# Kernel optimization log

Hardware: AMD Instinct MI355X
Metric: run time of the kernel (lower is better)

Reference implementation:

```python
import jax, jax.numpy as jnp
import numpy as np

B, L, D, H = 2, 2048, 2048, 16
HD = D // H  # head_dim = 128
EPS = 1e-5


def setup_inputs() -> dict:
    key = jax.random.key(0)
    ks = jax.random.split(key, 5)
    return {
        "x": jax.random.normal(ks[0], (B, L, D), dtype=jnp.float32),
        "Wq": jax.random.normal(ks[1], (D, D), dtype=jnp.float32) * (D ** -0.5),
        "Wk": jax.random.normal(ks[2], (D, D), dtype=jnp.float32) * (D ** -0.5),
        "Wv": jax.random.normal(ks[3], (D, D), dtype=jnp.float32) * (D ** -0.5),
        "gamma_logit": jax.random.normal(ks[4], (H,), dtype=jnp.float32),
        "gn_weight": jnp.ones((D,), dtype=jnp.float32),
        "gn_bias": jnp.zeros((D,), dtype=jnp.float32),
    }


def reference(x, Wq, Wk, Wv, gamma_logit, gn_weight, gn_bias):
    scale = HD ** -0.5
    # projections (torch Linear: y = x @ W.T)
    Q = jnp.einsum('bld,ed->ble', x, Wq).reshape(B, L, H, HD).transpose(0, 2, 1, 3)
    K = jnp.einsum('bld,ed->ble', x, Wk).reshape(B, L, H, HD).transpose(0, 2, 1, 3)
    V = jnp.einsum('bld,ed->ble', x, Wv).reshape(B, L, H, HD).transpose(0, 2, 1, 3)
    # causal exponential decay matrix D[h,i,j] = gamma_h^(i-j), lower-triangular
    pos = jnp.arange(L)
    dist = jnp.abs(pos[None, :] - pos[:, None]).astype(jnp.float32)  # [L,L]
    gamma = jax.nn.sigmoid(gamma_logit)  # [H]
    Dmat = jnp.tril(gamma[:, None, None] ** dist[None, :, :])  # [H,L,L]
    # decayed linear attention (no softmax)
    attn = jnp.einsum('bhid,bhjd->bhij', Q, K) * scale * Dmat[None]
    out = jnp.einsum('bhij,bhje->bhie', attn, V)  # [B,H,L,HD]
    out = out.transpose(0, 2, 1, 3)  # [B,L,H,HD]
    # GroupNorm: channels=D, groups=H, spatial=L -> normalize per (b,h) over (L,HD)
    mean = out.mean(axis=(1, 3), keepdims=True)
    var = out.var(axis=(1, 3), keepdims=True)
    y = (out - mean) * jax.lax.rsqrt(var + EPS)
    y = y * gn_weight.reshape(1, 1, H, HD) + gn_bias.reshape(1, 1, H, HD)
    return y.reshape(B, L, D)
```

## Files before the change

kernel.cpp:

```cpp
#include <hip/hip_runtime.h>
#include <hip/hip_bf16.h>
#include <math.h>

#define B_  2
#define L_  2048
#define D_  2048
#define H_  16
#define HD_ 128
#define EPS_ 1e-5f

typedef __attribute__((ext_vector_type(8)))  short short8;
typedef __attribute__((ext_vector_type(4)))  float f32x4;
typedef __attribute__((ext_vector_type(16))) float f32x16;

static __device__ inline unsigned short bfb(float x) {
    __hip_bfloat16 h = __float2bfloat16(x);
    unsigned short s;
    __builtin_memcpy(&s, &h, 2);
    return s;
}
static __device__ inline unsigned pk2(float a, float b) {
    return (unsigned)bfb(a) | ((unsigned)bfb(b) << 16);
}
static __device__ inline float bf2f(unsigned short u) {
    unsigned v = ((unsigned)u) << 16;
    float f;
    __builtin_memcpy(&f, &v, 4);
    return f;
}

static __device__ __forceinline__ void gld_lds16(const void* g, void* l) {
    __builtin_amdgcn_global_load_lds(
        (const __attribute__((address_space(1))) unsigned int*)g,
        (__attribute__((address_space(3))) unsigned int*)l,
        16, 0, 0);
}

#define XN4 2097152
#define WN4 1048576
#define TOT4 (XN4 + 3 * WN4)

__global__ __launch_bounds__(256) void cast4_kernel(
    const float* __restrict__ x,  const float* __restrict__ Wq,
    const float* __restrict__ Wk, const float* __restrict__ Wv,
    __hip_bfloat16* __restrict__ dst)
{
    int i = blockIdx.x * 256 + threadIdx.x;
    const int st = gridDim.x * 256;
    for (; i < TOT4; i += st) {
        const float* s;
        int off;
        if (i < XN4)                { s = x;  off = i; }
        else if (i < XN4 + WN4)     { s = Wq; off = i - XN4; }
        else if (i < XN4 + 2 * WN4) { s = Wk; off = i - XN4 - WN4; }
        else                        { s = Wv; off = i - XN4 - 2 * WN4; }
        float4 v = ((const float4*)s)[off];
        uint2 r;
        r.x = pk2(v.x, v.y);
        r.y = pk2(v.z, v.w);
        ((uint2*)dst)[i] = r;
    }
}

__global__ __launch_bounds__(256) void proj_bf16(
    const __hip_bfloat16* __restrict__ X,
    const __hip_bfloat16* __restrict__ Wqb, const __hip_bfloat16* __restrict__ Wkb,
    const __hip_bfloat16* __restrict__ Wvb,
    __hip_bfloat16* __restrict__ Qo, __hip_bfloat16* __restrict__ Ko,
    __hip_bfloat16* __restrict__ Vt, __hip_bfloat16* __restrict__ Kt)
{
    const __hip_bfloat16* W = (blockIdx.z == 0) ? Wqb : (blockIdx.z == 1 ? Wkb : Wvb);
    __hip_bfloat16*       O = (blockIdx.z == 0) ? Qo  : (blockIdx.z == 1 ? Ko  : Vt);

    __shared__ __align__(16) char Al[128 * 64 * 2];
    __shared__ __align__(16) char Bl[128 * 64 * 2];

    const int t  = threadIdx.x;
    const int w  = t >> 6, l = t & 63;
    const int li = l & 15, hi4 = l >> 4;
    const int wr = w >> 1, wcn = w & 1;
    const int m0 = blockIdx.y * 128;
    const int n0 = blockIdx.x * 128;

    const int srow = l >> 3;
    const int scol = ((l & 7) ^ (l >> 3)) * 8;

    f32x4 acc[4][4];
    #pragma unroll
    for (int i = 0; i < 4; ++i)
        #pragma unroll
        for (int j = 0; j < 4; ++j)
            #pragma unroll
            for (int r = 0; r < 4; ++r) acc[i][j][r] = 0.f;

    for (int k0 = 0; k0 < D_; k0 += 64) {
        if (k0) __syncthreads();
        #pragma unroll
        for (int c = 0; c < 4; ++c) {
            const int chunk = w * 4 + c;
            const int row   = chunk * 8 + srow;
            gld_lds16(X + (size_t)(m0 + row) * D_ + k0 + scol, Al + chunk * 1024);
            gld_lds16(W + (size_t)(n0 + row) * D_ + k0 + scol, Bl + chunk * 1024);
        }
        __syncthreads();

        #pragma unroll
        for (int s = 0; s < 2; ++s) {
            const int cbA = (s * 64 + hi4 * 16) ^ ((li & 7) << 4);
            short8 af[4], bf[4];
            #pragma unroll
            for (int mi = 0; mi < 4; ++mi)
                af[mi] = *(const short8*)(Al + (wr * 64 + mi * 16 + li) * 128 + cbA);
            #pragma unroll
            for (int ni = 0; ni < 4; ++ni)
                bf[ni] = *(const short8*)(Bl + (wcn * 64 + ni * 16 + li) * 128 + cbA);
            #pragma unroll
            for (int mi = 0; mi < 4; ++mi)
                #pragma unroll
                for (int ni = 0; ni < 4; ++ni)
                    acc[mi][ni] = __builtin_amdgcn_mfma_f32_16x16x32_bf16(
                        af[mi], bf[ni], acc[mi][ni], 0, 0, 0);
        }
    }

    if (blockIdx.z == 2) {
        #pragma unroll
        for (int mi = 0; mi < 4; ++mi) {
            #pragma unroll
            for (int ni = 0; ni < 4; ++ni) {
                const int n     = n0 + wcn * 64 + ni * 16 + li;
                const int mbase = m0 + wr * 64 + mi * 16 + hi4 * 4;
                const int b = mbase >> 11, ml = mbase & (L_ - 1);
                uint2 w2;
                w2.x = pk2(acc[mi][ni][0], acc[mi][ni][1]);
                w2.y = pk2(acc[mi][ni][2], acc[mi][ni][3]);
                *(uint2*)&O[((size_t)b * (H_ * HD_) + n) * L_ + ml] = w2;
            }
        }
    } else {
        #pragma unroll
        for (int mi = 0; mi < 4; ++mi) {
            #pragma unroll
            for (int ni = 0; ni < 4; ++ni) {
                const int n  = n0 + wcn * 64 + ni * 16 + li;
                const int h  = n >> 7, hd = n & (HD_ - 1);
                #pragma unroll
                for (int r = 0; r < 4; ++r) {
                    const int m = m0 + wr * 64 + mi * 16 + hi4 * 4 + r;
                    const int b = m >> 11, ml = m & (L_ - 1);
                    O[((size_t)(b * H_ + h) * L_ + ml) * HD_ + hd] =
                        __float2bfloat16(acc[mi][ni][r]);
                }
            }
        }
        if (blockIdx.z == 1 && Kt != nullptr) {
            #pragma unroll
            for (int mi = 0; mi < 4; ++mi) {
                #pragma unroll
                for (int ni = 0; ni < 4; ++ni) {
                    const int n     = n0 + wcn * 64 + ni * 16 + li;
                    const int mbase = m0 + wr * 64 + mi * 16 + hi4 * 4;
                    const int b = mbase >> 11, ml = mbase & (L_ - 1);
                    uint2 w2;
                    w2.x = pk2(acc[mi][ni][0], acc[mi][ni][1]);
                    w2.y = pk2(acc[mi][ni][2], acc[mi][ni][3]);
                    *(uint2*)&Kt[((size_t)b * (H_ * HD_) + n) * L_ + ml] = w2;
                }
            }
        }
    }
}

__global__ __launch_bounds__(256) void state_part(
    const __hip_bfloat16* __restrict__ KT, const __hip_bfloat16* __restrict__ VT,
    const float* __restrict__ gl, __hip_bfloat16* __restrict__ SpT)
{
    const int bid = blockIdx.x;
    const int bh  = bid & 31, c = bid >> 5;
    const int h   = bh & (H_ - 1);
    const int t   = threadIdx.x;
    const int w   = t >> 6, l = t & 63;
    const int li  = l & 31, hi = l >> 5;

    const float gamma = 1.f / (1.f + __expf(-gl[h]));
    const float lg2   = __log2f(gamma);

    __shared__ __align__(16) char Kl[32768];
    __shared__ __align__(16) char Vl[32768];

    const __hip_bfloat16* KTg = KT + (size_t)bh * (HD_ * L_);
    const __hip_bfloat16* VTg = VT + (size_t)bh * (HD_ * L_);
    const int gj = c * 128;
    const int srow4 = l >> 4, sslot = l & 15;

    #pragma unroll
    for (int cc = 0; cc < 8; ++cc) {
        const int ch = w * 8 + cc;
        const int r  = ch * 4 + srow4;
        const int sc = ((sslot ^ (r & 15)) * 8);
        gld_lds16(KTg + (size_t)r * L_ + gj + sc, Kl + ch * 1024);
        gld_lds16(VTg + (size_t)r * L_ + gj + sc, Vl + ch * 1024);
    }
    __syncthreads();

    f32x16 acc[4];
    #pragma unroll
    for (int cch = 0; cch < 4; ++cch)
        #pragma unroll
        for (int r = 0; r < 16; ++r) acc[cch][r] = 0.f;

    #pragma unroll
    for (int s = 0; s < 8; ++s) {
        const int boff = ((s * 2 + hi) ^ (li & 15)) << 4;
        short8 vraw = *(const short8*)(Vl + (w * 32 + li) * 256 + boff);
        short8 af;
        #pragma unroll
        for (int e = 0; e < 8; ++e) {
            const int jl = s * 16 + hi * 8 + e;
            const float f = bf2f((unsigned short)vraw[e]) *
                            exp2f(lg2 * (float)(127 - jl));
            af[e] = (short)bfb(f);
        }
        #pragma unroll
        for (int cch = 0; cch < 4; ++cch) {
            short8 bf = *(const short8*)(Kl + (cch * 32 + li) * 256 + boff);
            acc[cch] = __builtin_amdgcn_mfma_f32_32x32x16_bf16(af, bf, acc[cch], 0, 0, 0);
        }
    }

    __hip_bfloat16* Sp = SpT + (size_t)(bh * 16 + c) * 16384;
    #pragma unroll
    for (int cch = 0; cch < 4; ++cch)
        #pragma unroll
        for (int r = 0; r < 16; ++r) {
            const int d = w * 32 + (r & 3) + 8 * (r >> 2) + 4 * hi;
            Sp[(size_t)d * 128 + cch * 32 + li] = __float2bfloat16(acc[cch][r]);
        }
}

__global__ __launch_bounds__(256) void state_scan(
    const __hip_bfloat16* __restrict__ SpT, __hip_bfloat16* __restrict__ SbT,
    const float* __restrict__ gl)
{
    const int bh = blockIdx.x;
    const int h  = bh & (H_ - 1);
    const float gamma = 1.f / (1.f + __expf(-gl[h]));
    const float g128  = exp2f(__log2f(gamma) * 128.f);
    const int fid = blockIdx.y * 256 + threadIdx.x;

    float a0 = 0.f, a1 = 0.f, a2 = 0.f, a3 = 0.f;
    for (int c = 0; c < 16; ++c) {
        const size_t off = (size_t)(bh * 16 + c) * 16384 + (size_t)fid * 4;
        uint2 v = *(const uint2*)(SpT + off);
        a0 = g128 * a0 + bf2f((unsigned short)(v.x & 0xffff));
        a1 = g128 * a1 + bf2f((unsigned short)(v.x >> 16));
        a2 = g128 * a2 + bf2f((unsigned short)(v.y & 0xffff));
        a3 = g128 * a3 + bf2f((unsigned short)(v.y >> 16));
        uint2 o;
        o.x = pk2(a0, a1);
        o.y = pk2(a2, a3);
        *(uint2*)(SbT + off) = o;
    }
}

__global__ __launch_bounds__(256) void retn_kernel(
    const __hip_bfloat16* __restrict__ Qb, const __hip_bfloat16* __restrict__ Kb,
    const __hip_bfloat16* __restrict__ VT, const float* __restrict__ gl,
    float* __restrict__ out, float2* __restrict__ part,
    const __hip_bfloat16* __restrict__ SbT, int use_chunks)
{
    const int bid = blockIdx.x;
    const int mm  = bid >> 5;
    const int m   = use_chunks ? mm : ((mm < 8) ? (15 - mm) : (mm - 8));
    const int bh  = bid & 31;
    const int b   = bh >> 4, h = bh & (H_ - 1);
    const int t   = threadIdx.x;
    const int w   = t >> 6, l = t & 63;
    const int li  = l & 31, hi = l >> 5;

    const float gamma = 1.f / (1.f + __expf(-gl[h]));
    const float lg2   = __log2f(gamma);
    const float scale = 0.08838834764831845f;

    __shared__ __align__(16) char Klds[32768];
    __shared__ __align__(16) char Vlds[32768];
    __shared__ float rs[4], rq[4];

    const size_t base = (size_t)bh * (L_ * HD_);
    const __hip_bfloat16* VTg = VT + (size_t)bh * (HD_ * L_);
    const int i0 = m * 128 + w * 32;

    short8 qf[8];
    {
        const __hip_bfloat16* qrow = Qb + base + (size_t)(i0 + li) * HD_;
        #pragma unroll
        for (int s = 0; s < 8; ++s)
            qf[s] = *(const short8*)(qrow + s * 16 + hi * 8);
    }

    float df[16];
    #pragma unroll
    for (int r = 0; r < 16; ++r) {
        const int jl = (r & 3) + 8 * (r >> 2) + 4 * hi;
        df[r] = exp2f(lg2 * (float)(li - jl));
    }

    f32x16 acc[4];
    #pragma unroll
    for (int c = 0; c < 4; ++c)
        #pragma unroll
        for (int r = 0; r < 16; ++r) acc[c][r] = 0.f;

    const int srow4 = l >> 4;
    const int sslot = l & 15;

    if (use_chunks && m > 0) {
        const __hip_bfloat16* Sg = SbT + (size_t)(bh * 16 + (m - 1)) * 16384;
        #pragma unroll
        for (int cc = 0; cc < 8; ++cc) {
            const int ch = w * 8 + cc;
            const int r  = ch * 4 + srow4;
            const int sc = ((sslot ^ (r & 15)) * 8);
            gld_lds16(Sg + (size_t)r * 128 + sc, Klds + ch * 1024);
        }
        __syncthreads();
        #pragma unroll
        for (int s = 0; s < 8; ++s) {
            const int boff = ((s * 2 + hi) ^ (li & 15)) << 4;
            #pragma unroll
            for (int cch = 0; cch < 4; ++cch) {
                short8 sf = *(const short8*)(Klds + (cch * 32 + li) * 256 + boff);
                acc[cch] = __builtin_amdgcn_mfma_f32_32x32x16_bf16(
                    qf[s], sf, acc[cch], 0, 0, 0);
            }
        }
        #pragma unroll
        for (int r = 0; r < 16; ++r) {
            const int il = (r & 3) + 8 * (r >> 2) + 4 * hi + w * 32;
            const float fr = exp2f(lg2 * (float)(il + 1)) * scale;
            acc[0][r] *= fr; acc[1][r] *= fr; acc[2][r] *= fr; acc[3][r] *= fr;
        }
    }

    const int gj0 = use_chunks ? m * 128 : 0;
    for (int gj = gj0; gj <= m * 128; gj += 128) {
        __syncthreads();
        #pragma unroll
        for (int cc = 0; cc < 8; ++cc) {
            const int c  = w * 8 + cc;
            const int r  = c * 4 + srow4;
            const int sc = ((sslot ^ (r & 15)) * 8);
            gld_lds16(Kb + base + (size_t)(gj + r) * HD_ + sc, Klds + c * 1024);
            gld_lds16(VTg + (size_t)r * L_ + gj + sc,          Vlds + c * 1024);
        }
        __syncthreads();

        const int tmax = ((i0 - gj) >> 5) < 3 ? ((i0 - gj) >> 5) : 3;
        for (int jt = 0; jt <= tmax; ++jt) {
            const int j0 = gj + jt * 32;

            f32x16 c;
            #pragma unroll
            for (int r = 0; r < 16; ++r) c[r] = 0.f;
            #pragma unroll
            for (int s = 0; s < 8; ++s) {
                short8 kf = *(const short8*)(Klds + (jt * 32 + li) * 256 +
                                             (((s * 2 + hi) ^ (li & 15)) << 4));
                c = __builtin_amdgcn_mfma_f32_32x32x16_bf16(kf, qf[s], c, 0, 0, 0);
            }

            float p[16];
            const float bt = exp2f(lg2 * (float)(i0 - j0)) * scale;
            if (j0 == i0) {
                #pragma unroll
                for (int r = 0; r < 16; ++r) {
                    const int jl = (r & 3) + 8 * (r >> 2) + 4 * hi;
                    p[r] = (jl <= li) ? c[r] * (df[r] * bt) : 0.f;
                }
            } else {
                #pragma unroll
                for (int r = 0; r < 16; ++r) p[r] = c[r] * (df[r] * bt);
            }

            #pragma unroll
            for (int sl = 0; sl < 2; ++sl) {
                const int o = sl * 8;
                unsigned pk01 = pk2(p[o + 0], p[o + 1]);
                unsigned pk23 = pk2(p[o + 2], p[o + 3]);
                unsigned pk45 = pk2(p[o + 4], p[o + 5]);
                unsigned pk67 = pk2(p[o + 6], p[o + 7]);
                unsigned x01 = (unsigned)__shfl_xor((int)pk01, 32);
                unsigned x23 = (unsigned)__shfl_xor((int)pk23, 32);
                unsigned x45 = (unsigned)__shfl_xor((int)pk45, 32);
                unsigned x67 = (unsigned)__shfl_xor((int)pk67, 32);
                union { short8 v; unsigned u[4]; } pf;
                pf.u[0] = hi ? x45 : pk01;
                pf.u[1] = hi ? x67 : pk23;
                pf.u[2] = hi ? pk45 : x01;
                pf.u[3] = hi ? pk67 : x23;
                #pragma unroll
                for (int cch = 0; cch < 4; ++cch) {
                    short8 vf = *(const short8*)(Vlds + (cch * 32 + li) * 256 +
                                 (((jt * 4 + sl * 2 + hi) ^ (li & 15)) << 4));
                    acc[cch] = __builtin_amdgcn_mfma_f32_32x32x16_bf16(
                        pf.v, vf, acc[cch], 0, 0, 0);
                }
            }
        }
    }

    float s = 0.f, sq = 0.f;
    #pragma unroll
    for (int cch = 0; cch < 4; ++cch) {
        #pragma unroll
        for (int r = 0; r < 16; ++r) {
            const int row = (r & 3) + 8 * (r >> 2) + 4 * hi;
            const float v = acc[cch][r];
            out[(size_t)(b * L_ + i0 + row) * D_ + h * HD_ + cch * 32 + li] = v;
            s += v; sq += v * v;
        }
    }

    #pragma unroll
    for (int off = 32; off > 0; off >>= 1) {
        s  += __shfl_down(s, off);
        sq += __shfl_down(sq, off);
    }
    if (l == 0) { rs[w] = s; rq[w] = sq; }
    __syncthreads();
    if (t == 0)
        part[bh * 16 + m] = make_float2(rs[0] + rs[1] + rs[2] + rs[3],
                                        rq[0] + rq[1] + rq[2] + rq[3]);
}

__global__ __launch_bounds__(256) void gn_apply(
    float* __restrict__ out, const float2* __restrict__ part,
    const float* __restrict__ gw, const float* __restrict__ gb)
{
    const int bh = blockIdx.x, sl = blockIdx.y;
    const int b = bh >> 4, h = bh & (H_ - 1);
    const int t = threadIdx.x;

    float S = 0.f, SQ = 0.f;
    #pragma unroll
    for (int i = 0; i < 16; ++i) {
        float2 p = part[bh * 16 + i];
        S += p.x; SQ += p.y;
    }
    const float inv  = 1.f / (float)(L_ * HD_);
    const float mean = S * inv;
    float var = SQ * inv - mean * mean;
    if (var < 0.f) var = 0.f;
    const float rstd = rsqrtf(var + EPS_);

    #pragma unroll
    for (int it = 0; it < 4; ++it) {
        const int n  = it * 256 + t;
        const int ll = n >> 5, d4 = n & 31;
        const size_t idx = (size_t)(b * L_ + sl * 32 + ll) * D_ + h * HD_ + d4 * 4;
        float4 v = *(const float4*)&out[idx];
        const float4 w4 = *(const float4*)&gw[h * HD_ + d4 * 4];
        const float4 b4 = *(const float4*)&gb[h * HD_ + d4 * 4];
        v.x = (v.x - mean) * rstd * w4.x + b4.x;
        v.y = (v.y - mean) * rstd * w4.y + b4.y;
        v.z = (v.z - mean) * rstd * w4.z + b4.z;
        v.w = (v.w - mean) * rstd * w4.w + b4.w;
        *(float4*)&out[idx] = v;
    }
}

extern "C" void kernel_launch(void* const* d_in, const int* in_sizes, int n_in,
                              void* d_out, int out_size, void* d_ws, size_t ws_size,
                              hipStream_t stream) {
    const float* x  = (const float*)d_in[0];
    const float* Wq = (const float*)d_in[1];
    const float* Wk = (const float*)d_in[2];
    const float* Wv = (const float*)d_in[3];
    const float* gl = (const float*)d_in[4];
    const float* gw = (const float*)d_in[5];
    const float* gb = (const float*)d_in[6];
    float* out = (float*)d_out;

    __hip_bfloat16* ws = (__hip_bfloat16*)d_ws;
    __hip_bfloat16* xb  = ws;
    __hip_bfloat16* Wqb = xb  + 8388608;
    __hip_bfloat16* Wkb = Wqb + 4194304;
    __hip_bfloat16* Wvb = Wkb + 4194304;
    __hip_bfloat16* Qbf = Wvb + 4194304;
    __hip_bfloat16* Kbf = Qbf + 8388608;
    __hip_bfloat16* VTb = Kbf + 8388608;
    float2* part = (float2*)(VTb + 8388608);
    __hip_bfloat16* KTb = (__hip_bfloat16*)(part + 512);

    __hip_bfloat16* SpT = xb;
    __hip_bfloat16* SbT = Wqb;

    const int use_chunks = (ws_size >= 109056000ULL) ? 1 : 0;

    cast4_kernel<<<2048, 256, 0, stream>>>(x, Wq, Wk, Wv, xb);

    dim3 pgrid(D_ / 128, (B_ * L_) / 128, 3);
    proj_bf16<<<pgrid, 256, 0, stream>>>(xb, Wqb, Wkb, Wvb, Qbf, Kbf, VTb,
                                         use_chunks ? KTb : nullptr);

    if (use_chunks) {
        state_part<<<dim3(512), 256, 0, stream>>>(KTb, VTb, gl, SpT);
        state_scan<<<dim3(32, 16), 256, 0, stream>>>(SpT, SbT, gl);
    }

    retn_kernel<<<dim3(512), 256, 0, stream>>>(Qbf, Kbf, VTb, gl, out, part,
                                               use_chunks ? SbT : nullptr,
                                               use_chunks);

    gn_apply<<<dim3(32, 64), 256, 0, stream>>>(out, part, gw, gb);
}
```

Baseline: 189.1 us.

## Rewrite QKV projection as double-buffered 128x256 tile GEMM with interleaved prefetch

The projection kernel now runs as a single 1D grid of 768 blocks of 512 threads. Each block computes a 128x256 output tile over the concatenated Wq/Wk/Wv weights, which sit contiguously in the workspace. Tiles of the next two k-steps are loaded into double-buffered LDS while MFMAs run, using vmcnt waits, raw barriers and s_setprio. Blocks are remapped so neighbouring ones share weight tiles in cache. The aim is to hide global load latency and raise MFMA utilisation, at the cost of 96KB of LDS per block, which lowers occupancy.

```diff
diff --git a/kernel.cpp b/kernel.cpp
--- a/kernel.cpp
+++ b/kernel.cpp
@@ -8,6 +8,7 @@
 #define H_  16
 #define HD_ 128
 #define EPS_ 1e-5f
+#define NTK 32
 
 typedef __attribute__((ext_vector_type(8)))  short short8;
 typedef __attribute__((ext_vector_type(4)))  float f32x4;
@@ -62,28 +63,30 @@
     }
 }
 
-__global__ __launch_bounds__(256) void proj_bf16(
+__global__ __launch_bounds__(512) void proj8(
     const __hip_bfloat16* __restrict__ X,
-    const __hip_bfloat16* __restrict__ Wqb, const __hip_bfloat16* __restrict__ Wkb,
-    const __hip_bfloat16* __restrict__ Wvb,
+    const __hip_bfloat16* __restrict__ Wc,
     __hip_bfloat16* __restrict__ Qo, __hip_bfloat16* __restrict__ Ko,
-    __hip_bfloat16* __restrict__ Vt, __hip_bfloat16* __restrict__ Kt)
+    __hip_bfloat16* __restrict__ VT, __hip_bfloat16* __restrict__ KT)
 {
-    const __hip_bfloat16* W = (blockIdx.z == 0) ? Wqb : (blockIdx.z == 1 ? Wkb : Wvb);
-    __hip_bfloat16*       O = (blockIdx.z == 0) ? Qo  : (blockIdx.z == 1 ? Ko  : Vt);
-
-    __shared__ __align__(16) char Al[128 * 64 * 2];
-    __shared__ __align__(16) char Bl[128 * 64 * 2];
+    __shared__ __align__(16) char lds[98304];
 
     const int t  = threadIdx.x;
     const int w  = t >> 6, l = t & 63;
     const int li = l & 15, hi4 = l >> 4;
-    const int wr = w >> 1, wcn = w & 1;
-    const int m0 = blockIdx.y * 128;
-    const int n0 = blockIdx.x * 128;
+    const int wm = w >> 2, wn = w & 3;
+
+    const int bid = blockIdx.x;
+    const int wg  = (bid & 7) * 96 + (bid >> 3);
+    const int nt  = wg >> 5;
+    const int mt  = wg & 31;
+    const int m0  = mt * 128;
+    const int n0g = nt * 256;
 
     const int srow = l >> 3;
     const int scol = ((l & 7) ^ (l >> 3)) * 8;
+    const int ca0  = 2 * w;
+    const int cb0  = 4 * w;
 
     f32x4 acc[4][4];
     #pragma unroll
@@ -93,78 +96,136 @@
             #pragma unroll
             for (int r = 0; r < 4; ++r) acc[i][j][r] = 0.f;
 
-    for (int k0 = 0; k0 < D_; k0 += 64) {
-        if (k0) __syncthreads();
-        #pragma unroll
-        for (int c = 0; c < 4; ++c) {
-            const int chunk = w * 4 + c;
-            const int row   = chunk * 8 + srow;
-            gld_lds16(X + (size_t)(m0 + row) * D_ + k0 + scol, Al + chunk * 1024);
-            gld_lds16(W + (size_t)(n0 + row) * D_ + k0 + scol, Bl + chunk * 1024);
-        }
-        __syncthreads();
-
-        #pragma unroll
-        for (int s = 0; s < 2; ++s) {
-            const int cbA = (s * 64 + hi4 * 16) ^ ((li & 7) << 4);
-            short8 af[4], bf[4];
-            #pragma unroll
-            for (int mi = 0; mi < 4; ++mi)
-                af[mi] = *(const short8*)(Al + (wr * 64 + mi * 16 + li) * 128 + cbA);
-            #pragma unroll
-            for (int ni = 0; ni < 4; ++ni)
-                bf[ni] = *(const short8*)(Bl + (wcn * 64 + ni * 16 + li) * 128 + cbA);
-            #pragma unroll
-            for (int mi = 0; mi < 4; ++mi)
-                #pragma unroll
-                for (int ni = 0; ni < 4; ++ni)
-                    acc[mi][ni] = __builtin_amdgcn_mfma_f32_16x16x32_bf16(
-                        af[mi], bf[ni], acc[mi][ni], 0, 0, 0);
-        }
-    }
-
-    if (blockIdx.z == 2) {
-        #pragma unroll
-        for (int mi = 0; mi < 4; ++mi) {
-            #pragma unroll
-            for (int ni = 0; ni < 4; ++ni) {
-                const int n     = n0 + wcn * 64 + ni * 16 + li;
-                const int mbase = m0 + wr * 64 + mi * 16 + hi4 * 4;
+    auto STAGE_A = [&](int tt) {
+        char* Ab = lds + (tt & 1) * 16384;
+        char* Bb = lds + 32768 + (tt & 1) * 32768;
+        const size_t kc = (size_t)(tt * 64) + scol;
+        gld_lds16(X  + (size_t)(m0 + ca0 * 8 + srow) * D_ + kc,      Ab + ca0 * 1024);
+        gld_lds16(X  + (size_t)(m0 + ca0 * 8 + 8 + srow) * D_ + kc,  Ab + ca0 * 1024 + 1024);
+        gld_lds16(Wc + (size_t)(n0g + cb0 * 8 + srow) * D_ + kc,     Bb + cb0 * 1024);
+    };
+    auto STAGE_B = [&](int tt) {
+        char* Bb = lds + 32768 + (tt & 1) * 32768;
+        const size_t kc = (size_t)(tt * 64) + scol;
+        gld_lds16(Wc + (size_t)(n0g + (cb0 + 1) * 8 + srow) * D_ + kc, Bb + (cb0 + 1) * 1024);
+        gld_lds16(Wc + (size_t)(n0g + (cb0 + 2) * 8 + srow) * D_ + kc, Bb + (cb0 + 2) * 1024);
+        gld_lds16(Wc + (size_t)(n0g + (cb0 + 3) * 8 + srow) * D_ + kc, Bb + (cb0 + 3) * 1024);
+    };
+
+    STAGE_A(0); STAGE_B(0); STAGE_A(1); STAGE_B(1);
+
+    const int cbk0 = (hi4 * 16) ^ ((li & 7) << 4);
+    const int cbk1 = (64 + hi4 * 16) ^ ((li & 7) << 4);
+
+    #pragma unroll 2
+    for (int kt = 0; kt < NTK; ++kt) {
+        const char* Ab = lds + (kt & 1) * 16384;
+        const char* Bb = lds + 32768 + (kt & 1) * 32768;
+
+        if (kt < NTK - 1) asm volatile("s_waitcnt vmcnt(6)" ::: "memory");
+        else              asm volatile("s_waitcnt vmcnt(0)" ::: "memory");
+        __builtin_amdgcn_s_barrier();
+
+        short8 a0[4], b0[4], a1[4], b1[4];
+        #pragma unroll
+        for (int mf = 0; mf < 4; ++mf)
+            a0[mf] = *(const short8*)(Ab + (wm * 64 + mf * 16 + li) * 128 + cbk0);
+        #pragma unroll
+        for (int nf = 0; nf < 4; ++nf)
+            b0[nf] = *(const short8*)(Bb + (wn * 64 + nf * 16 + li) * 128 + cbk0);
+        __builtin_amdgcn_s_setprio(1);
+        #pragma unroll
+        for (int mf = 0; mf < 4; ++mf)
+            #pragma unroll
+            for (int nf = 0; nf < 2; ++nf)
+                acc[mf][nf] = __builtin_amdgcn_mfma_f32_16x16x32_bf16(
+                    a0[mf], b0[nf], acc[mf][nf], 0, 0, 0);
+        __builtin_amdgcn_s_setprio(0);
+
+        #pragma unroll
+        for (int mf = 0; mf < 4; ++mf)
+            a1[mf] = *(const short8*)(Ab + (wm * 64 + mf * 16 + li) * 128 + cbk1);
+        #pragma unroll
+        for (int nf = 0; nf < 4; ++nf)
+            b1[nf] = *(const short8*)(Bb + (wn * 64 + nf * 16 + li) * 128 + cbk1);
+        __builtin_amdgcn_s_setprio(1);
+        #pragma unroll
+        for (int mf = 0; mf < 4; ++mf)
+            #pragma unroll
+            for (int nf = 2; nf < 4; ++nf)
+                acc[mf][nf] = __builtin_amdgcn_mfma_f32_16x16x32_bf16(
+                    a0[mf], b0[nf], acc[mf][nf], 0, 0, 0);
+        __builtin_amdgcn_s_setprio(0);
+
+        asm volatile("s_waitcnt lgkmcnt(0)" ::: "memory");
+        __builtin_amdgcn_s_barrier();
+
+        if (kt < NTK - 2) STAGE_A(kt + 2);
+        __builtin_amdgcn_s_setprio(1);
+        #pragma unroll
+        for (int mf = 0; mf < 4; ++mf)
+            #pragma unroll
+            for (int nf = 0; nf < 2; ++nf)
+                acc[mf][nf] = __builtin_amdgcn_mfma_f32_16x16x32_bf16(
+                    a1[mf], b1[nf], acc[mf][nf], 0, 0, 0);
+        __builtin_amdgcn_s_setprio(0);
+
+        if (kt < NTK - 2) STAGE_B(kt + 2);
+        __builtin_amdgcn_s_setprio(1);
+        #pragma unroll
+        for (int mf = 0; mf < 4; ++mf)
+            #pragma unroll
+            for (int nf = 2; nf < 4; ++nf)
+                acc[mf][nf] = __builtin_amdgcn_mfma_f32_16x16x32_bf16(
+                    a1[mf], b1[nf], acc[mf][nf], 0, 0, 0);
+        __builtin_amdgcn_s_setprio(0);
+    }
+
+    const int zsel = n0g >> 11;
+    const int np   = n0g & (D_ - 1);
+    if (zsel == 2) {
+        #pragma unroll
+        for (int mf = 0; mf < 4; ++mf) {
+            #pragma unroll
+            for (int nf = 0; nf < 4; ++nf) {
+                const int n     = np + wn * 64 + nf * 16 + li;
+                const int mbase = m0 + wm * 64 + mf * 16 + hi4 * 4;
                 const int b = mbase >> 11, ml = mbase & (L_ - 1);
                 uint2 w2;
-                w2.x = pk2(acc[mi][ni][0], acc[mi][ni][1]);
-                w2.y = pk2(acc[mi][ni][2], acc[mi][ni][3]);
-                *(uint2*)&O[((size_t)b * (H_ * HD_) + n) * L_ + ml] = w2;
+                w2.x = pk2(acc[mf][nf][0], acc[mf][nf][1]);
+                w2.y = pk2(acc[mf][nf][2], acc[mf][nf][3]);
+                *(uint2*)&VT[((size_t)b * D_ + n) * L_ + ml] = w2;
             }
         }
     } else {
-        #pragma unroll
-        for (int mi = 0; mi < 4; ++mi) {
-            #pragma unroll
-            for (int ni = 0; ni < 4; ++ni) {
-                const int n  = n0 + wcn * 64 + ni * 16 + li;
+        __hip_bfloat16* O = zsel ? Ko : Qo;
+        #pragma unroll
+        for (int mf = 0; mf < 4; ++mf) {
+            #pragma unroll
+            for (int nf = 0; nf < 4; ++nf) {
+                const int n  = np + wn * 64 + nf * 16 + li;
                 const int h  = n >> 7, hd = n & (HD_ - 1);
                 #pragma unroll
                 for (int r = 0; r < 4; ++r) {
-                    const int m = m0 + wr * 64 + mi * 16 + hi4 * 4 + r;
+                    const int m = m0 + wm * 64 + mf * 16 + hi4 * 4 + r;
                     const int b = m >> 11, ml = m & (L_ - 1);
                     O[((size_t)(b * H_ + h) * L_ + ml) * HD_ + hd] =
-                        __float2bfloat16(acc[mi][ni][r]);
+                        __float2bfloat16(acc[mf][nf][r]);
                 }
             }
         }
-        if (blockIdx.z == 1 && Kt != nullptr) {
-            #pragma unroll
-            for (int mi = 0; mi < 4; ++mi) {
+        if (zsel == 1 && KT != nullptr) {
+            #pragma unroll
+            for (int mf = 0; mf < 4; ++mf) {
                 #pragma unroll
-                for (int ni = 0; ni < 4; ++ni) {
-                    const int n     = n0 + wcn * 64 + ni * 16 + li;
-                    const int mbase = m0 + wr * 64 + mi * 16 + hi4 * 4;
+                for (int nf = 0; nf < 4; ++nf) {
+                    const int n     = np + wn * 64 + nf * 16 + li;
+                    const int mbase = m0 + wm * 64 + mf * 16 + hi4 * 4;
                     const int b = mbase >> 11, ml = mbase & (L_ - 1);
                     uint2 w2;
-                    w2.x = pk2(acc[mi][ni][0], acc[mi][ni][1]);
-                    w2.y = pk2(acc[mi][ni][2], acc[mi][ni][3]);
-                    *(uint2*)&Kt[((size_t)b * (H_ * HD_) + n) * L_ + ml] = w2;
+                    w2.x = pk2(acc[mf][nf][0], acc[mf][nf][1]);
+                    w2.y = pk2(acc[mf][nf][2], acc[mf][nf][3]);
+                    *(uint2*)&KT[((size_t)b * D_ + n) * L_ + ml] = w2;
                 }
             }
         }
@@ -499,8 +560,7 @@
 
     cast4_kernel<<<2048, 256, 0, stream>>>(x, Wq, Wk, Wv, xb);
 
-    dim3 pgrid(D_ / 128, (B_ * L_) / 128, 3);
-    proj_bf16<<<pgrid, 256, 0, stream>>>(xb, Wqb, Wkb, Wvb, Qbf, Kbf, VTb,
+    proj8<<<dim3(768), 512, 0, stream>>>(xb, Wqb, Qbf, Kbf, VTb,
                                          use_chunks ? KTb : nullptr);
 
     if (use_chunks) {
```

New measurement: 184.5 us (median of 2 runs). 2.4% less time.

## Use 256x128 projection tiles over concatenated QKV weights with XCD-aware block mapping

Applied to the files above, without the earlier changes.

The projection GEMM is rewritten so each block computes a 256x128 tile, with every wave holding 8x4 MFMA accumulators. This doubles A-tile reuse and halves the B loads per output. The three weight matrices are treated as one concatenated 6144-row matrix (Wq, Wk, Wv sit contiguously in the workspace), and the grid becomes a 1D 768-block launch. Block ids are remapped so consecutive tiles land on the same XCD for L2 locality. The larger tile raises register and LDS use (launch_bounds 256,2) and cuts the block count, which may hurt occupancy.

```diff
diff --git a/kernel.cpp b/kernel.cpp
--- a/kernel.cpp
+++ b/kernel.cpp
@@ -62,32 +62,33 @@
     }
 }
 
-__global__ __launch_bounds__(256) void proj_bf16(
+__global__ __launch_bounds__(256, 2) void proj_fat(
     const __hip_bfloat16* __restrict__ X,
-    const __hip_bfloat16* __restrict__ Wqb, const __hip_bfloat16* __restrict__ Wkb,
-    const __hip_bfloat16* __restrict__ Wvb,
+    const __hip_bfloat16* __restrict__ Wc,
     __hip_bfloat16* __restrict__ Qo, __hip_bfloat16* __restrict__ Ko,
-    __hip_bfloat16* __restrict__ Vt, __hip_bfloat16* __restrict__ Kt)
+    __hip_bfloat16* __restrict__ VT, __hip_bfloat16* __restrict__ KT)
 {
-    const __hip_bfloat16* W = (blockIdx.z == 0) ? Wqb : (blockIdx.z == 1 ? Wkb : Wvb);
-    __hip_bfloat16*       O = (blockIdx.z == 0) ? Qo  : (blockIdx.z == 1 ? Ko  : Vt);
-
-    __shared__ __align__(16) char Al[128 * 64 * 2];
+    __shared__ __align__(16) char Al[256 * 64 * 2];
     __shared__ __align__(16) char Bl[128 * 64 * 2];
 
     const int t  = threadIdx.x;
     const int w  = t >> 6, l = t & 63;
     const int li = l & 15, hi4 = l >> 4;
-    const int wr = w >> 1, wcn = w & 1;
-    const int m0 = blockIdx.y * 128;
-    const int n0 = blockIdx.x * 128;
+    const int wm = w >> 1, wn = w & 1;
+
+    const int bid = blockIdx.x;
+    const int wg  = (bid & 7) * 96 + (bid >> 3);
+    const int mt  = wg & 15;
+    const int nt  = wg >> 4;
+    const int m0  = mt * 256;
+    const int n0g = nt * 128;
 
     const int srow = l >> 3;
     const int scol = ((l & 7) ^ (l >> 3)) * 8;
 
-    f32x4 acc[4][4];
-    #pragma unroll
-    for (int i = 0; i < 4; ++i)
+    f32x4 acc[8][4];
+    #pragma unroll
+    for (int i = 0; i < 8; ++i)
         #pragma unroll
         for (int j = 0; j < 4; ++j)
             #pragma unroll
@@ -96,75 +97,82 @@
     for (int k0 = 0; k0 < D_; k0 += 64) {
         if (k0) __syncthreads();
         #pragma unroll
-        for (int c = 0; c < 4; ++c) {
-            const int chunk = w * 4 + c;
-            const int row   = chunk * 8 + srow;
-            gld_lds16(X + (size_t)(m0 + row) * D_ + k0 + scol, Al + chunk * 1024);
-            gld_lds16(W + (size_t)(n0 + row) * D_ + k0 + scol, Bl + chunk * 1024);
+        for (int cc = 0; cc < 8; ++cc) {
+            const int c   = w * 8 + cc;
+            const int row = c * 8 + srow;
+            gld_lds16(X + (size_t)(m0 + row) * D_ + k0 + scol, Al + c * 1024);
+        }
+        #pragma unroll
+        for (int cc = 0; cc < 4; ++cc) {
+            const int c   = w * 4 + cc;
+            const int row = c * 8 + srow;
+            gld_lds16(Wc + (size_t)(n0g + row) * D_ + k0 + scol, Bl + c * 1024);
         }
         __syncthreads();
 
         #pragma unroll
         for (int s = 0; s < 2; ++s) {
-            const int cbA = (s * 64 + hi4 * 16) ^ ((li & 7) << 4);
-            short8 af[4], bf[4];
-            #pragma unroll
-            for (int mi = 0; mi < 4; ++mi)
-                af[mi] = *(const short8*)(Al + (wr * 64 + mi * 16 + li) * 128 + cbA);
-            #pragma unroll
-            for (int ni = 0; ni < 4; ++ni)
-                bf[ni] = *(const short8*)(Bl + (wcn * 64 + ni * 16 + li) * 128 + cbA);
-            #pragma unroll
-            for (int mi = 0; mi < 4; ++mi)
+            const int cb = (s * 64 + hi4 * 16) ^ ((li & 7) << 4);
+            short8 bfr[4];
+            #pragma unroll
+            for (int nf = 0; nf < 4; ++nf)
+                bfr[nf] = *(const short8*)(Bl + (wn * 64 + nf * 16 + li) * 128 + cb);
+            #pragma unroll
+            for (int mf = 0; mf < 8; ++mf) {
+                short8 af = *(const short8*)(Al + (wm * 128 + mf * 16 + li) * 128 + cb);
                 #pragma unroll
-                for (int ni = 0; ni < 4; ++ni)
-                    acc[mi][ni] = __builtin_amdgcn_mfma_f32_16x16x32_bf16(
-                        af[mi], bf[ni], acc[mi][ni], 0, 0, 0);
-        }
-    }
-
-    if (blockIdx.z == 2) {
-        #pragma unroll
-        for (int mi = 0; mi < 4; ++mi) {
-            #pragma unroll
-            for (int ni = 0; ni < 4; ++ni) {
-                const int n     = n0 + wcn * 64 + ni * 16 + li;
-                const int mbase = m0 + wr * 64 + mi * 16 + hi4 * 4;
+                for (int nf = 0; nf < 4; ++nf)
+                    acc[mf][nf] = __builtin_amdgcn_mfma_f32_16x16x32_bf16(
+                        af, bfr[nf], acc[mf][nf], 0, 0, 0);
+            }
+        }
+    }
+
+    const int zsel = n0g >> 11;
+    const int np   = n0g & (D_ - 1);
+    if (zsel == 2) {
+        #pragma unroll
+        for (int mf = 0; mf < 8; ++mf) {
+            #pragma unroll
+            for (int nf = 0; nf < 4; ++nf) {
+                const int n     = np + wn * 64 + nf * 16 + li;
+                const int mbase = m0 + wm * 128 + mf * 16 + hi4 * 4;
                 const int b = mbase >> 11, ml = mbase & (L_ - 1);
                 uint2 w2;
-                w2.x = pk2(acc[mi][ni][0], acc[mi][ni][1]);
-                w2.y = pk2(acc[mi][ni][2], acc[mi][ni][3]);
-                *(uint2*)&O[((size_t)b * (H_ * HD_) + n) * L_ + ml] = w2;
+                w2.x = pk2(acc[mf][nf][0], acc[mf][nf][1]);
+                w2.y = pk2(acc[mf][nf][2], acc[mf][nf][3]);
+                *(uint2*)&VT[((size_t)b * D_ + n) * L_ + ml] = w2;
             }
         }
     } else {
-        #pragma unroll
-        for (int mi = 0; mi < 4; ++mi) {
-            #pragma unroll
-            for (int ni = 0; ni < 4; ++ni) {
-                const int n  = n0 + wcn * 64 + ni * 16 + li;
+        __hip_bfloat16* O = zsel ? Ko : Qo;
+        #pragma unroll
+        for (int mf = 0; mf < 8; ++mf) {
+            #pragma unroll
+            for (int nf = 0; nf < 4; ++nf) {
+                const int n  = np + wn * 64 + nf * 16 + li;
                 const int h  = n >> 7, hd = n & (HD_ - 1);
                 #pragma unroll
                 for (int r = 0; r < 4; ++r) {
-                    const int m = m0 + wr * 64 + mi * 16 + hi4 * 4 + r;
+                    const int m = m0 + wm * 128 + mf * 16 + hi4 * 4 + r;
                     const int b = m >> 11, ml = m & (L_ - 1);
                     O[((size_t)(b * H_ + h) * L_ + ml) * HD_ + hd] =
-                        __float2bfloat16(acc[mi][ni][r]);
+                        __float2bfloat16(acc[mf][nf][r]);
                 }
             }
         }
-        if (blockIdx.z == 1 && Kt != nullptr) {
-            #pragma unroll
-            for (int mi = 0; mi < 4; ++mi) {
+        if (zsel == 1 && KT != nullptr) {
+            #pragma unroll
+            for (int mf = 0; mf < 8; ++mf) {
                 #pragma unroll
-                for (int ni = 0; ni < 4; ++ni) {
-                    const int n     = n0 + wcn * 64 + ni * 16 + li;
-                    const int mbase = m0 + wr * 64 + mi * 16 + hi4 * 4;
+                for (int nf = 0; nf < 4; ++nf) {
+                    const int n     = np + wn * 64 + nf * 16 + li;
+                    const int mbase = m0 + wm * 128 + mf * 16 + hi4 * 4;
                     const int b = mbase >> 11, ml = mbase & (L_ - 1);
                     uint2 w2;
-                    w2.x = pk2(acc[mi][ni][0], acc[mi][ni][1]);
-                    w2.y = pk2(acc[mi][ni][2], acc[mi][ni][3]);
-                    *(uint2*)&Kt[((size_t)b * (H_ * HD_) + n) * L_ + ml] = w2;
+                    w2.x = pk2(acc[mf][nf][0], acc[mf][nf][1]);
+                    w2.y = pk2(acc[mf][nf][2], acc[mf][nf][3]);
+                    *(uint2*)&KT[((size_t)b * D_ + n) * L_ + ml] = w2;
                 }
             }
         }
@@ -499,9 +507,8 @@
 
     cast4_kernel<<<2048, 256, 0, stream>>>(x, Wq, Wk, Wv, xb);
 
-    dim3 pgrid(D_ / 128, (B_ * L_) / 128, 3);
-    proj_bf16<<<pgrid, 256, 0, stream>>>(xb, Wqb, Wkb, Wvb, Qbf, Kbf, VTb,
-                                         use_chunks ? KTb : nullptr);
+    proj_fat<<<dim3(768), 256, 0, stream>>>(xb, Wqb, Qbf, Kbf, VTb,
+                                            use_chunks ? KTb : nullptr);
 
     if (use_chunks) {
         state_part<<<dim3(512), 256, 0, stream>>>(KTb, VTb, gl, SpT);
```

After: 198.4 us. 1.05x slower.
